# Optimization experiments

Measured on AMD Instinct MI355X. Metric: run time of the kernel, lower is better.

## Reference

```python
import jax, jax.numpy as jnp
import numpy as np

B, T, D, H, DK = 4, 2048, 1024, 16, 64  # batch, seq, d_model, heads, head_dim (dk==dv)


def setup_inputs() -> dict:
    key = jax.random.key(0)
    ks = jax.random.split(key, 9)
    s = 0.02
    return {
        "q": jax.random.normal(ks[0], (B, T, D), jnp.float32),
        "k": jax.random.normal(ks[1], (B, T, D), jnp.float32),
        "v": jax.random.normal(ks[2], (B, T, D), jnp.float32),
        "attn_mask": jax.random.randint(ks[3], (B, T, T), 0, 2, jnp.int32),
        "Wq": jax.random.normal(ks[4], (D, H * DK), jnp.float32) * s,
        "bq": jnp.zeros((H * DK,), jnp.float32),
        "Wk": jax.random.normal(ks[5], (D, H * DK), jnp.float32) * s,
        "bk": jnp.zeros((H * DK,), jnp.float32),
        "Wv": jax.random.normal(ks[6], (D, H * DK), jnp.float32) * s,
        "bv": jnp.zeros((H * DK,), jnp.float32),
        "Wo": jax.random.normal(ks[7], (H * DK, D), jnp.float32) * s,
        "bo": jnp.zeros((D,), jnp.float32),
        "gamma": jnp.ones((D,), jnp.float32),
        "beta": jnp.zeros((D,), jnp.float32),
    }


def reference(q, k, v, attn_mask, Wq, bq, Wk, bk, Wv, bv, Wo, bo, gamma, beta):
    Bn, Tq, _ = q.shape
    Tk = k.shape[1]
    residual = q
    mask = attn_mask.astype(jnp.float32)  # (B, Tq, Tk), multiplicative

    qh = (q @ Wq + bq).reshape(Bn, Tq, H, DK)
    kh = (k @ Wk + bk).reshape(Bn, Tk, H, DK)
    vh = (v @ Wv + bv).reshape(Bn, Tk, H, DK)

    # NOTE: original applies NO 1/sqrt(d) scaling (temper is computed but unused)
    attn = jnp.einsum("bqhd,bkhd->hbqk", qh, kh)  # (H, B, Tq, Tk)
    attn = attn * mask[None]                      # multiplicative mask
    attn = attn - jnp.max(attn)                   # GLOBAL max subtract (whole tensor)
    attn = jnp.exp(attn) * mask[None]             # re-mask after exp
    attn = attn / (jnp.sum(attn, axis=-1, keepdims=True) + 1e-15)
    # dropout is identity at inference

    out = jnp.einsum("hbqk,bkhd->bqhd", attn, vh).reshape(Bn, Tq, H * DK)
    out = out @ Wo + bo  # (B, Tq, D); dropout identity

    x = out + residual
    mu = jnp.mean(x, axis=-1, keepdims=True)
    var = jnp.mean((x - mu) ** 2, axis=-1, keepdims=True)
    return (x - mu) / jnp.sqrt(var + 1e-5) * gamma + beta
```

## Files before the change

kernel.cpp:

```cpp
#include <hip/hip_runtime.h>
#include <stdint.h>

#define T_ 2048
#define H_ 16

typedef __attribute__((ext_vector_type(8))) short bf16x8;
typedef __attribute__((ext_vector_type(4))) float f32x4;

__device__ __forceinline__ unsigned short f2bf(float x){
  union { float f; uint32_t u; } v; v.f = x;
  uint32_t r = v.u + 0x7FFFu + ((v.u >> 16) & 1u);
  return (unsigned short)(r >> 16);
}

__device__ __forceinline__ void g2l16(const void* g, void* l){
  __builtin_amdgcn_global_load_lds(
      (const __attribute__((address_space(1))) void*)g,
      (__attribute__((address_space(3))) void*)l, 16, 0, 0);
}

__global__ __launch_bounds__(256) void cvt3_kernel(
    const float* __restrict__ q, const float* __restrict__ k, const float* __restrict__ v,
    unsigned short* __restrict__ oq, unsigned short* __restrict__ ok, unsigned short* __restrict__ ov){
  const long NG = (long)8*1024*1024/4;
  long g = (long)blockIdx.x*256 + threadIdx.x;
  const float* s; unsigned short* d;
  if (g < NG){ s=q; d=oq; }
  else if (g < 2*NG){ s=k; d=ok; g-=NG; }
  else { s=v; d=ov; g-=2*NG; }
  long i = g*4;
  float4 val = *(const float4*)(s+i);
  ushort4 r;
  r.x=f2bf(val.x); r.y=f2bf(val.y); r.z=f2bf(val.z); r.w=f2bf(val.w);
  *(ushort4*)(d+i) = r;
}

__global__ __launch_bounds__(256) void wt_kernel(
    const float* __restrict__ W0, const float* __restrict__ W1,
    const float* __restrict__ W2, const float* __restrict__ W3,
    unsigned short* __restrict__ out){
  __shared__ unsigned short t[64][72];
  const float* W = (blockIdx.z==0)?W0:(blockIdx.z==1)?W1:(blockIdx.z==2)?W2:W3;
  const float sc = (blockIdx.z==0) ? 1.44269504f : 1.0f;
  unsigned short* o = out + (size_t)blockIdx.z*1024*1024;
  int k0 = blockIdx.x*64, n0 = blockIdx.y*64;
  int tid = threadIdx.x;
  int i = tid>>2, cs = (tid&3)*16;
  const float* src = W + (size_t)(k0+i)*1024 + n0 + cs;
  #pragma unroll
  for (int c=0;c<16;c+=4){
    float4 vv = *(const float4*)(src + c);
    t[i][cs+c+0]=f2bf(vv.x*sc); t[i][cs+c+1]=f2bf(vv.y*sc);
    t[i][cs+c+2]=f2bf(vv.z*sc); t[i][cs+c+3]=f2bf(vv.w*sc);
  }
  __syncthreads();
  int j = tid>>2; int ks = (tid&3)*16;
  __align__(16) unsigned short buf[16];
  #pragma unroll
  for (int c=0;c<16;c++) buf[c] = t[ks+c][j];
  unsigned short* dst = o + (size_t)(n0+j)*1024 + k0 + ks;
  *(uint4*)dst = *(const uint4*)(buf);
  *(uint4*)(dst+8) = *(const uint4*)(buf+8);
}

__global__ __launch_bounds__(256) void pack_mask_kernel(
    const int* __restrict__ mask, unsigned long long* __restrict__ mw){
  int wid = threadIdx.x>>6, lane = threadIdx.x&63;
  long r = (long)blockIdx.x*4 + wid;
  const int* mrow = mask + r*2048;
  unsigned long long* orow = mw + r*32;
  for (int kk=0; kk<32; kk++){
    int vv = mrow[kk*64 + lane];
    unsigned long long bal = __ballot(vv != 0);
    if (lane==0) orow[kk] = bal;
  }
}

template<int FUSED>
__device__ __forceinline__ void gemm_body(
    const unsigned short* __restrict__ A,
    const unsigned short* __restrict__ Bt,
    const float* __restrict__ bias, float bscale,
    const float* __restrict__ resid,
    void* __restrict__ Cout,
    unsigned short* sA, unsigned short* sB){
  const int K = 1024;
  int tid = threadIdx.x;
  int wid = tid>>6, lane = tid&63;
  int ln = lane&15, qd = lane>>4;
  int wr = wid>>1, wc = wid&1;
  long m0 = (long)blockIdx.y*128;
  long n0 = (long)blockIdx.x*128;
  f32x4 acc[4][4] = {};
  for (int k0=0; k0<K; k0+=64){
    __syncthreads();
    #pragma unroll
    for (int s=0;s<4;s++){
      int G = s*256 + tid;
      int mm = G>>3, cc = G&7;
      g2l16(A  + (m0+mm)*(long)K + k0 + ((cc^(mm&7))<<3),
            (char*)sA + (size_t)G*16);
      g2l16(Bt + (n0+mm)*(long)K + k0 + ((cc^(mm&7))<<3),
            (char*)sB + (size_t)G*16);
    }
    __syncthreads();
    #pragma unroll
    for (int ks=0;ks<2;ks++){
      bf16x8 af[4], bfv[4];
      #pragma unroll
      for (int i=0;i<4;i++){
        int rowa = wr*64 + i*16 + ln;
        af[i]  = *(const bf16x8*)(sA + rowa*64 + (((ks*4+qd)^(rowa&7))<<3));
        int rowb = wc*64 + i*16 + ln;
        bfv[i] = *(const bf16x8*)(sB + rowb*64 + (((ks*4+qd)^(rowb&7))<<3));
      }
      #pragma unroll
      for (int i=0;i<4;i++)
        #pragma unroll
        for (int j=0;j<4;j++)
          acc[i][j] = __builtin_amdgcn_mfma_f32_16x16x32_bf16(af[i], bfv[j], acc[i][j], 0,0,0);
    }
  }
  long gm0 = m0 + wr*64, gn0 = n0 + wc*64;
  #pragma unroll
  for (int j=0;j<4;j++){
    long gn = gn0 + j*16 + ln;
    float bv = bias[gn]*bscale;
    #pragma unroll
    for (int i=0;i<4;i++){
      long gm = gm0 + i*16 + qd*4;
      #pragma unroll
      for (int r=0;r<4;r++){
        float val = acc[i][j][r] + bv;
        if (FUSED){
          ((float*)Cout)[(gm+r)*1024 + gn] = val + resid[(gm+r)*1024 + gn];
        } else {
          ((unsigned short*)Cout)[(gm+r)*1024 + gn] = f2bf(val);
        }
      }
    }
  }
}

__global__ __launch_bounds__(256,2) void gemm_qkv(
    const unsigned short* __restrict__ Aq, const unsigned short* __restrict__ Ak,
    const unsigned short* __restrict__ Av, const unsigned short* __restrict__ Wt,
    const float* __restrict__ bq, const float* __restrict__ bk, const float* __restrict__ bv,
    unsigned short* __restrict__ Cq, unsigned short* __restrict__ Ck,
    unsigned short* __restrict__ Cv){
  __shared__ unsigned short sA[128*64];
  __shared__ unsigned short sB[128*64];
  int z = blockIdx.z;
  const unsigned short* A  = (z==0)?Aq:(z==1)?Ak:Av;
  const unsigned short* Bt = Wt + (size_t)z*1024*1024;
  const float* bias        = (z==0)?bq:(z==1)?bk:bv;
  unsigned short* C        = (z==0)?Cq:(z==1)?Ck:Cv;
  float bscale             = (z==0)?1.44269504f:1.0f;
  gemm_body<0>(A, Bt, bias, bscale, nullptr, C, sA, sB);
}

__global__ __launch_bounds__(256,2) void gemm_out(
    const unsigned short* __restrict__ A, const unsigned short* __restrict__ Bt,
    const float* __restrict__ bias, const float* __restrict__ resid,
    float* __restrict__ Cout){
  __shared__ unsigned short sA[128*64];
  __shared__ unsigned short sB[128*64];
  gemm_body<1>(A, Bt, bias, 1.0f, resid, Cout, sA, sB);
}

__global__ __launch_bounds__(256) void vt_kernel(
    const unsigned short* __restrict__ vh, unsigned short* __restrict__ vt){
  __shared__ unsigned short t[64][72];
  int t0 = blockIdx.x*64;
  int bh = blockIdx.y;
  int b = bh>>4, h = bh&15;
  int tid = threadIdx.x;
  int i = tid>>2, cs=(tid&3)*16;
  const unsigned short* src = vh + ((long)b*T_ + t0 + i)*1024 + h*64 + cs;
  *(bf16x8*)&t[i][cs]   = *(const bf16x8*)(src);
  *(bf16x8*)&t[i][cs+8] = *(const bf16x8*)(src+8);
  __syncthreads();
  int j = tid>>2; int ks=(tid&3)*16;
  __align__(16) unsigned short buf[16];
  #pragma unroll
  for (int c=0;c<16;c++){
    int p = ks + c;
    int keyloc = (p&3)*16 + (p>>2);
    buf[c] = t[keyloc][j];
  }
  unsigned short* dst = vt + ((long)bh*64 + j)*2048 + t0 + ks;
  *(uint4*)dst = *(const uint4*)buf;
  *(uint4*)(dst+8) = *(const uint4*)(buf+8);
}

__global__ __launch_bounds__(128,2) void attn_kernel(
    const unsigned short* __restrict__ qh,
    const unsigned short* __restrict__ kh,
    const unsigned short* __restrict__ vt,
    const unsigned long long* __restrict__ mw,
    unsigned short* __restrict__ aout){
  __shared__ unsigned short kS[64*64];
  __shared__ unsigned short vS[64*64];
  __shared__ unsigned short pS[2][64][72];
  int tid=threadIdx.x, wid=tid>>6, lane=tid&63;
  int ln=lane&15, qd=lane>>4;
  int q0 = blockIdx.x*128;
  int bh = blockIdx.y, b = bh>>4, h = bh&15;
  int wq0 = q0 + wid*64;

  bf16x8 qf[4][2];
  const unsigned short* qbase = qh + ((long)b*T_ + wq0)*1024 + h*64 + qd*8;
  #pragma unroll
  for (int rg=0;rg<4;rg++){
    qf[rg][0] = *(const bf16x8*)(qbase + (size_t)(rg*16+ln)*1024);
    qf[rg][1] = *(const bf16x8*)(qbase + (size_t)(rg*16+ln)*1024 + 32);
  }
  f32x4 oacc[4][4] = {};
  f32x4 lsum[4] = {};
  bf16x8 ones;
  #pragma unroll
  for (int i=0;i<8;i++) ones[i] = (short)0x3F80;

  const unsigned short* khB  = kh + ((long)b*T_)*1024 + h*64;
  const unsigned short* vtB2 = vt + ((long)bh*64)*2048;
  const unsigned long long* mwB = mw + ((long)(b*T_ + wq0 + qd*4))*32;

  for (int t=0; t<32; t++){
    __syncthreads();
    #pragma unroll
    for (int s=0;s<4;s++){
      int G = s*128 + tid;
      int ii = G>>3, cc = G&7;
      g2l16(khB  + ((long)(t*64+ii))*1024 + ((cc^(ii&7))<<3), (char*)kS + (size_t)G*16);
      g2l16(vtB2 + (long)ii*2048 + t*64   + ((cc^(ii&7))<<3), (char*)vS + (size_t)G*16);
    }
    unsigned long long mb[4][4];
    #pragma unroll
    for (int rg=0;rg<4;rg++)
      #pragma unroll
      for (int r=0;r<4;r++)
        mb[rg][r] = mwB[(size_t)(rg*16+r)*32 + t];
    __syncthreads();

    bf16x8 kb[2][4];
    #pragma unroll
    for (int ks=0;ks<2;ks++)
      #pragma unroll
      for (int nt=0;nt<4;nt++){
        int row = nt*16+ln;
        kb[ks][nt] = *(const bf16x8*)(kS + row*64 + (((ks*4+qd)^(row&7))<<3));
      }
    #pragma unroll
    for (int rg=0;rg<4;rg++){
      f32x4 sa[4];
      #pragma unroll
      for (int nt=0;nt<4;nt++){
        f32x4 z = {-20.f,-20.f,-20.f,-20.f};
        z = __builtin_amdgcn_mfma_f32_16x16x32_bf16(qf[rg][0], kb[0][nt], z, 0,0,0);
        z = __builtin_amdgcn_mfma_f32_16x16x32_bf16(qf[rg][1], kb[1][nt], z, 0,0,0);
        sa[nt]=z;
      }
      #pragma unroll
      for (int r=0;r<4;r++){
        unsigned long long w = mb[rg][r] >> ln;
        unsigned int lo = (unsigned int)w, hi = (unsigned int)(w>>32);
        union { uint32_t u; float f; } t0v,t1v,t2v,t3v;
        t0v.u = ((lo      &1u)-1u) & 0xC47A0000u;
        t1v.u = (((lo>>16)&1u)-1u) & 0xC47A0000u;
        t2v.u = ((hi      &1u)-1u) & 0xC47A0000u;
        t3v.u = (((hi>>16)&1u)-1u) & 0xC47A0000u;
        float p0 = __builtin_amdgcn_exp2f(sa[0][r] + t0v.f);
        float p1 = __builtin_amdgcn_exp2f(sa[1][r] + t1v.f);
        float p2 = __builtin_amdgcn_exp2f(sa[2][r] + t2v.f);
        float p3 = __builtin_amdgcn_exp2f(sa[3][r] + t3v.f);
        unsigned a0 = __float_as_uint(p0) + 0x8000u;
        unsigned a1 = __float_as_uint(p1) + 0x8000u;
        unsigned a2 = __float_as_uint(p2) + 0x8000u;
        unsigned a3 = __float_as_uint(p3) + 0x8000u;
        unsigned loP = __builtin_amdgcn_perm(a1, a0, 0x07060302u);
        unsigned hiP = __builtin_amdgcn_perm(a3, a2, 0x07060302u);
        *(unsigned long long*)&pS[wid][rg*16+qd*4+r][ln*4] =
            ((unsigned long long)hiP<<32) | (unsigned long long)loP;
      }
    }
    asm volatile("s_waitcnt lgkmcnt(0)" ::: "memory");

    #pragma unroll
    for (int c=0;c<2;c++){
      bf16x8 vb[4];
      #pragma unroll
      for (int d=0;d<4;d++){
        int row = d*16+ln;
        vb[d] = *(const bf16x8*)(vS + row*64 + (((c*4+qd)^(row&7))<<3));
      }
      #pragma unroll
      for (int rg=0;rg<4;rg++){
        bf16x8 pa = *(const bf16x8*)&pS[wid][rg*16+ln][c*32+qd*8];
        #pragma unroll
        for (int d=0;d<4;d++)
          oacc[rg][d] = __builtin_amdgcn_mfma_f32_16x16x32_bf16(pa, vb[d], oacc[rg][d], 0,0,0);
        lsum[rg] = __builtin_amdgcn_mfma_f32_16x16x32_bf16(pa, ones, lsum[rg], 0,0,0);
      }
    }
  }

  #pragma unroll
  for (int rg=0;rg<4;rg++){
    float linv[4];
    #pragma unroll
    for (int r=0;r<4;r++) linv[r] = (lsum[rg][r]>0.f)?(1.f/lsum[rg][r]):0.f;
    long rowb = (long)b*T_ + wq0 + rg*16 + qd*4;
    #pragma unroll
    for (int d=0;d<4;d++)
      #pragma unroll
      for (int r=0;r<4;r++)
        aout[(rowb+r)*1024 + h*64 + d*16 + ln] = f2bf(oacc[rg][d][r]*linv[r]);
  }
}

__global__ __launch_bounds__(256) void ln_kernel(const float* __restrict__ x,
    const float* __restrict__ gamma, const float* __restrict__ beta, float* __restrict__ out){
  __shared__ float red[8];
  long row = blockIdx.x;
  const float* xr = x + row*1024;
  int tid = threadIdx.x;
  float4 v = *(const float4*)(xr + tid*4);
  float s = v.x+v.y+v.z+v.w;
  float sq = v.x*v.x+v.y*v.y+v.z*v.z+v.w*v.w;
  #pragma unroll
  for (int off=1; off<64; off<<=1){
    s  += __shfl_xor(s,off,64);
    sq += __shfl_xor(sq,off,64);
  }
  int wid=tid>>6, lane=tid&63;
  if (lane==0){ red[wid]=s; red[4+wid]=sq; }
  __syncthreads();
  float S  = red[0]+red[1]+red[2]+red[3];
  float SQ = red[4]+red[5]+red[6]+red[7];
  float mu = S*(1.0f/1024.0f);
  float var = SQ*(1.0f/1024.0f) - mu*mu;
  float rstd = rsqrtf(var + 1e-5f);
  float4 g  = *(const float4*)(gamma + tid*4);
  float4 be = *(const float4*)(beta + tid*4);
  float4 o;
  o.x=(v.x-mu)*rstd*g.x+be.x;
  o.y=(v.y-mu)*rstd*g.y+be.y;
  o.z=(v.z-mu)*rstd*g.z+be.z;
  o.w=(v.w-mu)*rstd*g.w+be.w;
  *(float4*)(out + row*1024 + tid*4) = o;
}

extern "C" void kernel_launch(void* const* d_in, const int* in_sizes, int n_in,
                              void* d_out, int out_size, void* d_ws, size_t ws_size,
                              hipStream_t stream){
  const float* q = (const float*)d_in[0];
  const float* k = (const float*)d_in[1];
  const float* v = (const float*)d_in[2];
  const int*   mask = (const int*)d_in[3];
  const float* Wq = (const float*)d_in[4];
  const float* bq = (const float*)d_in[5];
  const float* Wk = (const float*)d_in[6];
  const float* bk = (const float*)d_in[7];
  const float* Wv = (const float*)d_in[8];
  const float* bv = (const float*)d_in[9];
  const float* Wo = (const float*)d_in[10];
  const float* bo = (const float*)d_in[11];
  const float* gamma = (const float*)d_in[12];
  const float* beta  = (const float*)d_in[13];
  float* out = (float*)d_out;
  char* ws = (char*)d_ws;
  const size_t MB = 1024*1024;
  unsigned short*     Wt  = (unsigned short*)(ws + 0);
  unsigned long long* mw  = (unsigned long long*)(ws + 8*MB);
  unsigned short*     qhB = (unsigned short*)(ws + 10*MB);
  unsigned short*     khB = (unsigned short*)(ws + 26*MB);
  unsigned short*     vhB = (unsigned short*)(ws + 42*MB);
  unsigned short*     qbf = (unsigned short*)(ws + 58*MB);
  unsigned short*     kbf = (unsigned short*)(ws + 74*MB);
  unsigned short*     vbf = (unsigned short*)(ws + 90*MB);
  unsigned short*     vtB  = vbf;
  unsigned short*     aout = qbf;
  float*              xbuf = (float*)(ws + 10*MB);

  cvt3_kernel<<<24576,256,0,stream>>>(q,k,v,qbf,kbf,vbf);
  wt_kernel<<<dim3(16,16,4),256,0,stream>>>(Wq,Wk,Wv,Wo,Wt);
  pack_mask_kernel<<<2048,256,0,stream>>>(mask, mw);
  gemm_qkv<<<dim3(8,64,3),256,0,stream>>>(qbf,kbf,vbf, Wt, bq,bk,bv, qhB,khB,vhB);
  vt_kernel<<<dim3(32,64),256,0,stream>>>(vhB, vtB);
  attn_kernel<<<dim3(16,64),128,0,stream>>>(qhB, khB, vtB, mw, aout);
  gemm_out<<<dim3(8,64),256,0,stream>>>(aout, Wt+3*1024*1024, bo, q, xbuf);
  ln_kernel<<<8192,256,0,stream>>>(xbuf, gamma, beta, out);
}
```

Before: 477.0 us.

## Double-buffer attention K/V tiles, fuse prep kernels, simplify mask application

Merges the three preprocessing kernels (input bf16 conversion, weight transpose, mask bit-packing) into one launch that dispatches on block index, removing two kernel launches. The attention kernel now double-buffers its K and V shared-memory tiles, prefetching tile t+1 while computing on tile t, with a single waitcnt+barrier per iteration. The mask is now applied by bitwise-zeroing the packed bf16 probabilities instead of adding a large negative bias before exp2, and the round-to-nearest add before truncation to bf16 is dropped. Double buffering doubles K/V LDS use, which may affect occupancy, and the missing rounding slightly changes numerics.

```diff
diff --git a/kernel.cpp b/kernel.cpp
--- a/kernel.cpp
+++ b/kernel.cpp
@@ -19,60 +19,62 @@
       (__attribute__((address_space(3))) void*)l, 16, 0, 0);
 }
 
-__global__ __launch_bounds__(256) void cvt3_kernel(
+__global__ __launch_bounds__(256) void prep_kernel(
     const float* __restrict__ q, const float* __restrict__ k, const float* __restrict__ v,
-    unsigned short* __restrict__ oq, unsigned short* __restrict__ ok, unsigned short* __restrict__ ov){
-  const long NG = (long)8*1024*1024/4;
-  long g = (long)blockIdx.x*256 + threadIdx.x;
-  const float* s; unsigned short* d;
-  if (g < NG){ s=q; d=oq; }
-  else if (g < 2*NG){ s=k; d=ok; g-=NG; }
-  else { s=v; d=ov; g-=2*NG; }
-  long i = g*4;
-  float4 val = *(const float4*)(s+i);
-  ushort4 r;
-  r.x=f2bf(val.x); r.y=f2bf(val.y); r.z=f2bf(val.z); r.w=f2bf(val.w);
-  *(ushort4*)(d+i) = r;
-}
-
-__global__ __launch_bounds__(256) void wt_kernel(
+    unsigned short* __restrict__ oq, unsigned short* __restrict__ ok, unsigned short* __restrict__ ov,
     const float* __restrict__ W0, const float* __restrict__ W1,
     const float* __restrict__ W2, const float* __restrict__ W3,
-    unsigned short* __restrict__ out){
+    unsigned short* __restrict__ wt_out,
+    const int* __restrict__ mask, unsigned long long* __restrict__ mw){
   __shared__ unsigned short t[64][72];
-  const float* W = (blockIdx.z==0)?W0:(blockIdx.z==1)?W1:(blockIdx.z==2)?W2:W3;
-  const float sc = (blockIdx.z==0) ? 1.44269504f : 1.0f;
-  unsigned short* o = out + (size_t)blockIdx.z*1024*1024;
-  int k0 = blockIdx.x*64, n0 = blockIdx.y*64;
+  int bx = blockIdx.x;
   int tid = threadIdx.x;
-  int i = tid>>2, cs = (tid&3)*16;
-  const float* src = W + (size_t)(k0+i)*1024 + n0 + cs;
-  #pragma unroll
-  for (int c=0;c<16;c+=4){
-    float4 vv = *(const float4*)(src + c);
-    t[i][cs+c+0]=f2bf(vv.x*sc); t[i][cs+c+1]=f2bf(vv.y*sc);
-    t[i][cs+c+2]=f2bf(vv.z*sc); t[i][cs+c+3]=f2bf(vv.w*sc);
-  }
-  __syncthreads();
-  int j = tid>>2; int ks = (tid&3)*16;
-  __align__(16) unsigned short buf[16];
-  #pragma unroll
-  for (int c=0;c<16;c++) buf[c] = t[ks+c][j];
-  unsigned short* dst = o + (size_t)(n0+j)*1024 + k0 + ks;
-  *(uint4*)dst = *(const uint4*)(buf);
-  *(uint4*)(dst+8) = *(const uint4*)(buf+8);
-}
-
-__global__ __launch_bounds__(256) void pack_mask_kernel(
-    const int* __restrict__ mask, unsigned long long* __restrict__ mw){
-  int wid = threadIdx.x>>6, lane = threadIdx.x&63;
-  long r = (long)blockIdx.x*4 + wid;
-  const int* mrow = mask + r*2048;
-  unsigned long long* orow = mw + r*32;
-  for (int kk=0; kk<32; kk++){
-    int vv = mrow[kk*64 + lane];
-    unsigned long long bal = __ballot(vv != 0);
-    if (lane==0) orow[kk] = bal;
+  if (bx < 24576){
+    const long NG = (long)8*1024*1024/4;
+    long g = (long)bx*256 + tid;
+    const float* s; unsigned short* d;
+    if (g < NG){ s=q; d=oq; }
+    else if (g < 2*NG){ s=k; d=ok; g-=NG; }
+    else { s=v; d=ov; g-=2*NG; }
+    long i = g*4;
+    float4 val = *(const float4*)(s+i);
+    ushort4 r;
+    r.x=f2bf(val.x); r.y=f2bf(val.y); r.z=f2bf(val.z); r.w=f2bf(val.w);
+    *(ushort4*)(d+i) = r;
+  } else if (bx < 25600){
+    int wb = bx - 24576;
+    int z = wb >> 8, rem = wb & 255;
+    const float* W = (z==0)?W0:(z==1)?W1:(z==2)?W2:W3;
+    const float sc = (z==0) ? 1.44269504f : 1.0f;
+    unsigned short* o = wt_out + (size_t)z*1024*1024;
+    int k0 = (rem&15)*64, n0 = (rem>>4)*64;
+    int i = tid>>2, cs = (tid&3)*16;
+    const float* src = W + (size_t)(k0+i)*1024 + n0 + cs;
+    #pragma unroll
+    for (int c=0;c<16;c+=4){
+      float4 vv = *(const float4*)(src + c);
+      t[i][cs+c+0]=f2bf(vv.x*sc); t[i][cs+c+1]=f2bf(vv.y*sc);
+      t[i][cs+c+2]=f2bf(vv.z*sc); t[i][cs+c+3]=f2bf(vv.w*sc);
+    }
+    __syncthreads();
+    int j = tid>>2; int ks = (tid&3)*16;
+    __align__(16) unsigned short buf[16];
+    #pragma unroll
+    for (int c=0;c<16;c++) buf[c] = t[ks+c][j];
+    unsigned short* dst = o + (size_t)(n0+j)*1024 + k0 + ks;
+    *(uint4*)dst = *(const uint4*)(buf);
+    *(uint4*)(dst+8) = *(const uint4*)(buf+8);
+  } else {
+    int pb = bx - 25600;
+    int wid = tid>>6, lane = tid&63;
+    long r = (long)pb*4 + wid;
+    const int* mrow = mask + r*2048;
+    unsigned long long* orow = mw + r*32;
+    for (int kk=0; kk<32; kk++){
+      int vv = mrow[kk*64 + lane];
+      unsigned long long bal = __ballot(vv != 0);
+      if (lane==0) orow[kk] = bal;
+    }
   }
 }
 
@@ -193,14 +195,26 @@
   *(uint4*)(dst+8) = *(const uint4*)(buf+8);
 }
 
+__device__ __forceinline__ void attn_stage(
+    const unsigned short* khB, const unsigned short* vtB2, int t,
+    unsigned short* kSb, unsigned short* vSb, int tid){
+  #pragma unroll
+  for (int s=0;s<4;s++){
+    int G = s*128 + tid;
+    int ii = G>>3, cc = G&7;
+    g2l16(khB  + ((long)(t*64+ii))*1024 + ((cc^(ii&7))<<3), (char*)kSb + (size_t)G*16);
+    g2l16(vtB2 + (long)ii*2048 + t*64   + ((cc^(ii&7))<<3), (char*)vSb + (size_t)G*16);
+  }
+}
+
 __global__ __launch_bounds__(128,2) void attn_kernel(
     const unsigned short* __restrict__ qh,
     const unsigned short* __restrict__ kh,
     const unsigned short* __restrict__ vt,
     const unsigned long long* __restrict__ mw,
     unsigned short* __restrict__ aout){
-  __shared__ unsigned short kS[64*64];
-  __shared__ unsigned short vS[64*64];
+  __shared__ unsigned short kS[2][64*64];
+  __shared__ unsigned short vS[2][64*64];
   __shared__ unsigned short pS[2][64][72];
   int tid=threadIdx.x, wid=tid>>6, lane=tid&63;
   int ln=lane&15, qd=lane>>4;
@@ -225,22 +239,22 @@
   const unsigned short* vtB2 = vt + ((long)bh*64)*2048;
   const unsigned long long* mwB = mw + ((long)(b*T_ + wq0 + qd*4))*32;
 
+  attn_stage(khB, vtB2, 0, kS[0], vS[0], tid);
+
   for (int t=0; t<32; t++){
-    __syncthreads();
-    #pragma unroll
-    for (int s=0;s<4;s++){
-      int G = s*128 + tid;
-      int ii = G>>3, cc = G&7;
-      g2l16(khB  + ((long)(t*64+ii))*1024 + ((cc^(ii&7))<<3), (char*)kS + (size_t)G*16);
-      g2l16(vtB2 + (long)ii*2048 + t*64   + ((cc^(ii&7))<<3), (char*)vS + (size_t)G*16);
-    }
+    int buf = t & 1;
+    asm volatile("s_waitcnt vmcnt(0) lgkmcnt(0)\n\ts_barrier" ::: "memory");
+    if (t < 31)
+      attn_stage(khB, vtB2, t+1, kS[buf^1], vS[buf^1], tid);
     unsigned long long mb[4][4];
     #pragma unroll
     for (int rg=0;rg<4;rg++)
       #pragma unroll
       for (int r=0;r<4;r++)
         mb[rg][r] = mwB[(size_t)(rg*16+r)*32 + t];
-    __syncthreads();
+
+    const unsigned short* kSb = kS[buf];
+    const unsigned short* vSb = vS[buf];
 
     bf16x8 kb[2][4];
     #pragma unroll
@@ -248,7 +262,7 @@
       #pragma unroll
       for (int nt=0;nt<4;nt++){
         int row = nt*16+ln;
-        kb[ks][nt] = *(const bf16x8*)(kS + row*64 + (((ks*4+qd)^(row&7))<<3));
+        kb[ks][nt] = *(const bf16x8*)(kSb + row*64 + (((ks*4+qd)^(row&7))<<3));
       }
     #pragma unroll
     for (int rg=0;rg<4;rg++){
@@ -264,21 +278,14 @@
       for (int r=0;r<4;r++){
         unsigned long long w = mb[rg][r] >> ln;
         unsigned int lo = (unsigned int)w, hi = (unsigned int)(w>>32);
-        union { uint32_t u; float f; } t0v,t1v,t2v,t3v;
-        t0v.u = ((lo      &1u)-1u) & 0xC47A0000u;
-        t1v.u = (((lo>>16)&1u)-1u) & 0xC47A0000u;
-        t2v.u = ((hi      &1u)-1u) & 0xC47A0000u;
-        t3v.u = (((hi>>16)&1u)-1u) & 0xC47A0000u;
-        float p0 = __builtin_amdgcn_exp2f(sa[0][r] + t0v.f);
-        float p1 = __builtin_amdgcn_exp2f(sa[1][r] + t1v.f);
-        float p2 = __builtin_amdgcn_exp2f(sa[2][r] + t2v.f);
-        float p3 = __builtin_amdgcn_exp2f(sa[3][r] + t3v.f);
-        unsigned a0 = __float_as_uint(p0) + 0x8000u;
-        unsigned a1 = __float_as_uint(p1) + 0x8000u;
-        unsigned a2 = __float_as_uint(p2) + 0x8000u;
-        unsigned a3 = __float_as_uint(p3) + 0x8000u;
-        unsigned loP = __builtin_amdgcn_perm(a1, a0, 0x07060302u);
-        unsigned hiP = __builtin_amdgcn_perm(a3, a2, 0x07060302u);
+        float p0 = __builtin_amdgcn_exp2f(sa[0][r]);
+        float p1 = __builtin_amdgcn_exp2f(sa[1][r]);
+        float p2 = __builtin_amdgcn_exp2f(sa[2][r]);
+        float p3 = __builtin_amdgcn_exp2f(sa[3][r]);
+        unsigned loP = __builtin_amdgcn_perm(__float_as_uint(p1), __float_as_uint(p0), 0x07060302u);
+        unsigned hiP = __builtin_amdgcn_perm(__float_as_uint(p3), __float_as_uint(p2), 0x07060302u);
+        loP &= (lo & 0x00010001u) * 0xFFFFu;
+        hiP &= (hi & 0x00010001u) * 0xFFFFu;
         *(unsigned long long*)&pS[wid][rg*16+qd*4+r][ln*4] =
             ((unsigned long long)hiP<<32) | (unsigned long long)loP;
       }
@@ -291,7 +298,7 @@
       #pragma unroll
       for (int d=0;d<4;d++){
         int row = d*16+ln;
-        vb[d] = *(const bf16x8*)(vS + row*64 + (((c*4+qd)^(row&7))<<3));
+        vb[d] = *(const bf16x8*)(vSb + row*64 + (((c*4+qd)^(row&7))<<3));
       }
       #pragma unroll
       for (int rg=0;rg<4;rg++){
@@ -382,9 +389,7 @@
   unsigned short*     aout = qbf;
   float*              xbuf = (float*)(ws + 10*MB);
 
-  cvt3_kernel<<<24576,256,0,stream>>>(q,k,v,qbf,kbf,vbf);
-  wt_kernel<<<dim3(16,16,4),256,0,stream>>>(Wq,Wk,Wv,Wo,Wt);
-  pack_mask_kernel<<<2048,256,0,stream>>>(mask, mw);
+  prep_kernel<<<27648,256,0,stream>>>(q,k,v,qbf,kbf,vbf, Wq,Wk,Wv,Wo, Wt, mask, mw);
   gemm_qkv<<<dim3(8,64,3),256,0,stream>>>(qbf,kbf,vbf, Wt, bq,bk,bv, qhB,khB,vhB);
   vt_kernel<<<dim3(32,64),256,0,stream>>>(vhB, vtB);
   attn_kernel<<<dim3(16,64),128,0,stream>>>(qhB, khB, vtB, mw, aout);
```

Result: no change. 483.6 us (+1.4%).
